# Kernel optimization log

Measured on AMD Instinct MI355X. Metric: run time of the kernel, lower is better.

## Reference

```python
import jax, jax.numpy as jnp
import numpy as np

B, L, T, D, H, DH = 8, 1024, 1024, 768, 12, 64
SPATIAL_DIM = 5


def setup_inputs() -> dict:
    key = jax.random.key(0)
    ks = jax.random.split(key, 12)
    scale = 1.0 / np.sqrt(D)
    inp = {
        "q": jax.random.normal(ks[0], (B, L, D), dtype=jnp.float32),
        "k": jax.random.normal(ks[1], (B, T, D), dtype=jnp.float32),
        "v": jax.random.normal(ks[2], (B, T, D), dtype=jnp.float32),
        "pairwise_locs": jax.random.normal(ks[3], (B, L, T, SPATIAL_DIM), dtype=jnp.float32),
        # last 64 key positions are padding in every batch row (never all-True)
        "key_padding_mask": jnp.broadcast_to(jnp.arange(T) >= T - 64, (B, T)),
        "Wq": jax.random.normal(ks[4], (D, H * DH), dtype=jnp.float32) * scale,
        "bq": jnp.zeros((H * DH,), dtype=jnp.float32),
        "Wk": jax.random.normal(ks[5], (D, H * DH), dtype=jnp.float32) * scale,
        "bk": jnp.zeros((H * DH,), dtype=jnp.float32),
        "Wv": jax.random.normal(ks[6], (D, H * DH), dtype=jnp.float32) * scale,
        "bv": jnp.zeros((H * DH,), dtype=jnp.float32),
        "Wo": jax.random.normal(ks[7], (H * DH, D), dtype=jnp.float32) * scale,
        "bo": jnp.zeros((D,), dtype=jnp.float32),
    }
    return inp


def reference(q, k, v, pairwise_locs, key_padding_mask, Wq, bq, Wk, bk, Wv, bv, Wo, bo):
    # pairwise_locs is accepted but unused in this forward path (as in the source).
    b, l, _ = q.shape
    t = k.shape[1]
    qh = (q @ Wq + bq).reshape(b, l, H, DH)  # b l h d
    kh = (k @ Wk + bk).reshape(b, t, H, DH)  # b t h d
    vh = (v @ Wv + bv).reshape(b, t, H, DH)  # b t h d
    attn = jnp.einsum('blhd,bthd->bhlt', qh, kh) / jnp.sqrt(jnp.float32(DH))
    attn = jnp.where(key_padding_mask[:, None, None, :], -jnp.inf, attn)
    fused_attn = jax.nn.softmax(attn, axis=-1)
    out = jnp.einsum('bhlt,bthd->blhd', fused_attn, vh).reshape(b, l, H * DH)
    return out @ Wo + bo  # dropout is identity in eval mode
```

## Files before the change

### kernel.cpp

```cpp
#include <hip/hip_runtime.h>
#include <hip/hip_bf16.h>
#include <cstdint>
#include <cstddef>
#include <cmath>

#define NB 8
#define NL 1024
#define NT 1024
#define ND 768
#define NH 12
#define NDH 64
#define NM (NB*NL)

typedef short short8 __attribute__((ext_vector_type(8)));
typedef unsigned short ushort4v __attribute__((ext_vector_type(4)));
typedef unsigned int uint4v __attribute__((ext_vector_type(4)));
typedef unsigned int uint2v __attribute__((ext_vector_type(2)));
typedef float f32x4 __attribute__((ext_vector_type(4)));
typedef float float4v __attribute__((ext_vector_type(4)));

__device__ __forceinline__ unsigned short f2bf(float f) {
  union { __hip_bfloat16 h; unsigned short u; } cv;
  cv.h = __float2bfloat16(f);
  return cv.u;
}
__device__ __forceinline__ unsigned pk2(float lo, float hi) {
  return (unsigned)f2bf(lo) | ((unsigned)f2bf(hi) << 16);
}
__device__ __forceinline__ f32x4 vmax4(f32x4 a, f32x4 b) {
  f32x4 r;
  r[0] = fmaxf(a[0], b[0]); r[1] = fmaxf(a[1], b[1]);
  r[2] = fmaxf(a[2], b[2]); r[3] = fmaxf(a[3], b[3]);
  return r;
}
__device__ __forceinline__ void gll16(const void* g, void* l) {
  __builtin_amdgcn_global_load_lds(
      (const __attribute__((address_space(1))) unsigned int*)g,
      (__attribute__((address_space(3))) unsigned int*)l, 16, 0, 0);
}

__global__ __launch_bounds__(128) void maskbits_kernel(
    const unsigned int* __restrict__ mask, unsigned long long* __restrict__ mb) {
  const int id = threadIdx.x;
  const unsigned int* src = mask + (size_t)(id >> 4) * NT + (id & 15) * 64;
  unsigned long long m = 0;
  for (int j = 0; j < 64; j++) m |= (unsigned long long)(src[j] != 0u) << j;
  mb[id] = m;
}

__global__ __launch_bounds__(256) void wt_kernel(
    const float* __restrict__ W0, const float* __restrict__ W1,
    const float* __restrict__ W2, const float* __restrict__ W3,
    unsigned short* __restrict__ Wt) {
  __shared__ float tile[32][33];
  const float* W = blockIdx.z == 0 ? W0 : blockIdx.z == 1 ? W1 : blockIdx.z == 2 ? W2 : W3;
  const int k0 = blockIdx.x * 32, n0 = blockIdx.y * 32;
  const int tx = threadIdx.x & 31, ty = threadIdx.x >> 5;
  for (int r = ty; r < 32; r += 8) tile[r][tx] = W[(size_t)(k0 + r) * ND + n0 + tx];
  __syncthreads();
  unsigned short* out = Wt + (size_t)blockIdx.z * ND * ND;
  for (int r = ty; r < 32; r += 8) out[(size_t)(n0 + r) * ND + k0 + tx] = f2bf(tile[tx][r]);
}

template<int MODE>
__global__ __launch_bounds__(256) void gemm_kernel(
    const float* __restrict__ Af0, const float* __restrict__ Af1,
    const float* __restrict__ Af2, const unsigned short* __restrict__ Ab,
    const unsigned short* __restrict__ Wt,
    const float* __restrict__ bias0, const float* __restrict__ bias1,
    const float* __restrict__ bias2,
    unsigned short* __restrict__ outb0, unsigned short* __restrict__ outb1,
    unsigned short* __restrict__ outb2, float* __restrict__ outf) {
  __shared__ __align__(16) unsigned short As[128 * 64];
  __shared__ __align__(16) unsigned short Bs[128 * 64];
  const int tid = threadIdx.x, lane = tid & 63, w = tid >> 6;
  const int c = lane & 15, g = lane >> 4;
  const int wrow = w & 1, wcol = w >> 1;
  const int l8 = lane >> 3, l7 = lane & 7, csw = l7 ^ l8;
  const int mbase = blockIdx.x * 128, nbase = blockIdx.y * 128;
  const int z = (MODE == 0) ? blockIdx.z : 3;

  const float* Af = (MODE == 0) ? (z == 0 ? Af0 : z == 1 ? Af1 : Af2) : nullptr;
  const unsigned short* Bt = Wt + (size_t)z * ND * ND;
  const float* bias = (MODE == 0) ? (z == 0 ? bias0 : z == 1 ? bias1 : bias2) : bias0;

  f32x4 acc[4][4];
#pragma unroll
  for (int m = 0; m < 4; m++)
#pragma unroll
    for (int n = 0; n < 4; n++) acc[m][n] = (f32x4){0.f, 0.f, 0.f, 0.f};

  for (int k0 = 0; k0 < ND; k0 += 64) {
    if (MODE == 0) {
#pragma unroll
      for (int i = 0; i < 4; i++) {
        int id = i * 256 + tid;
        int r = id >> 3, cc = id & 7;
        const float* src = &Af[(size_t)(mbase + r) * ND + k0 + cc * 8];
        float4v x0 = *(const float4v*)src;
        float4v x1 = *(const float4v*)(src + 4);
        uint4v y = {pk2(x0[0], x0[1]), pk2(x0[2], x0[3]),
                    pk2(x1[0], x1[1]), pk2(x1[2], x1[3])};
        *(uint4v*)&As[r * 64 + ((cc ^ (r & 7)) * 8)] = y;
      }
    } else {
#pragma unroll
      for (int it = 0; it < 4; it++) {
        int r = it * 32 + w * 8 + l8;
        gll16(&Ab[(size_t)(mbase + r) * ND + k0 + csw * 8], &As[(it * 32 + w * 8) * 64]);
      }
    }
#pragma unroll
    for (int it = 0; it < 4; it++) {
      int r = it * 32 + w * 8 + l8;
      gll16(&Bt[(size_t)(nbase + r) * ND + k0 + csw * 8], &Bs[(it * 32 + w * 8) * 64]);
    }
    __syncthreads();

#pragma unroll
    for (int ks = 0; ks < 2; ks++) {
      short8 a[4], b[4];
#pragma unroll
      for (int m = 0; m < 4; m++) {
        int r = wrow * 64 + m * 16 + c;
        a[m] = *(const short8*)&As[r * 64 + (((ks * 4 + g) ^ (c & 7)) * 8)];
      }
#pragma unroll
      for (int n = 0; n < 4; n++) {
        int r = wcol * 64 + n * 16 + c;
        b[n] = *(const short8*)&Bs[r * 64 + (((ks * 4 + g) ^ (c & 7)) * 8)];
      }
      if (MODE == 0 && z == 2) {
#pragma unroll
        for (int m = 0; m < 4; m++)
#pragma unroll
          for (int n = 0; n < 4; n++)
            acc[m][n] = __builtin_amdgcn_mfma_f32_16x16x32_bf16(a[m], b[n], acc[m][n], 0, 0, 0);
      } else {
#pragma unroll
        for (int m = 0; m < 4; m++)
#pragma unroll
          for (int n = 0; n < 4; n++)
            acc[m][n] = __builtin_amdgcn_mfma_f32_16x16x32_bf16(b[n], a[m], acc[m][n], 0, 0, 0);
      }
    }
    __syncthreads();
  }

  if (MODE == 0 && z == 2) {
#pragma unroll
    for (int n = 0; n < 4; n++) {
      const int col = nbase + wcol * 64 + n * 16 + c;
      const float bv = bias[col];
      const int h = col >> 6, dd = col & 63;
#pragma unroll
      for (int m = 0; m < 4; m++) {
        const int r0 = mbase + wrow * 64 + m * 16 + g * 4;
        const int bb = r0 >> 10, t = r0 & (NT - 1);
        ushort4v y;
#pragma unroll
        for (int j = 0; j < 4; j++) y[j] = f2bf(acc[m][n][j] + bv);
        *(ushort4v*)&outb2[((size_t)(bb * NH + h) * NDH + dd) * NT + t] = y;
      }
    }
  } else {
    const float scale = (MODE == 0 && z == 0) ? 0.125f * 1.44269504f : 1.0f;
    unsigned short* outb = (MODE == 0) ? (z == 0 ? outb0 : outb1) : nullptr;
#pragma unroll
    for (int n = 0; n < 4; n++) {
      const int colb = nbase + wcol * 64 + n * 16 + g * 4;
      float4v bv4 = *(const float4v*)&bias[colb];
#pragma unroll
      for (int m = 0; m < 4; m++) {
        const int row = mbase + wrow * 64 + m * 16 + c;
        if (MODE == 3) {
          float4v y;
#pragma unroll
          for (int j = 0; j < 4; j++) y[j] = acc[m][n][j] + bv4[j];
          *(float4v*)&outf[(size_t)row * ND + colb] = y;
        } else {
          ushort4v y;
#pragma unroll
          for (int j = 0; j < 4; j++) y[j] = f2bf((acc[m][n][j] + bv4[j]) * scale);
          *(ushort4v*)&outb[(size_t)row * ND + colb] = y;
        }
      }
    }
  }
}

__global__ __launch_bounds__(256) void attn_kernel(
    const unsigned short* __restrict__ qh, const unsigned short* __restrict__ kh,
    const unsigned short* __restrict__ vhT, const unsigned long long* __restrict__ maskbits,
    unsigned short* __restrict__ ao) {
  __shared__ __align__(16) unsigned short Ks[2][64 * 64];
  __shared__ __align__(16) unsigned short Vs[2][64 * 64];
  __shared__ __align__(16) unsigned short Ps[4][32 * 32];
  const int tid = threadIdx.x, lane = tid & 63, w = tid >> 6;
  const int c = lane & 15, g = lane >> 4;
  const int l8 = lane >> 3, l7 = lane & 7;
  const int swz4 = (c & 3) ^ ((c >> 2) & 3);
  const int qb = blockIdx.x * 128;
  const int b = blockIdx.y / NH, h = blockIdx.y % NH;
  const size_t kbase = (size_t)b * NT * ND + h * NDH;
  const size_t vbase = (size_t)(b * NH + h) * NDH * NT;

  const unsigned mwsrc = ((const unsigned*)maskbits)[(size_t)b * 32 + (lane & 31)];

  short8 aq[2][2];
#pragma unroll
  for (int half = 0; half < 2; half++) {
    size_t qrow = (size_t)(b * NL + qb + w * 32 + half * 16 + c) * ND + h * NDH;
#pragma unroll
    for (int ks = 0; ks < 2; ks++)
      aq[half][ks] = *(const short8*)&qh[qrow + ks * 32 + g * 8];
  }

  f32x4 o[2][4], lrv[2];
#pragma unroll
  for (int half = 0; half < 2; half++) {
    lrv[half] = (f32x4){0.f, 0.f, 0.f, 0.f};
#pragma unroll
    for (int f = 0; f < 4; f++) o[half][f] = (f32x4){0.f, 0.f, 0.f, 0.f};
  }
  float mr[2] = {-1e30f, -1e30f};

#pragma unroll
  for (int it = 0; it < 2; it++) {
    int r = w * 16 + it * 8 + l8;
    int cs = l7 ^ (r & 7);
    gll16(&kh[kbase + (size_t)r * ND + cs * 8], &Ks[0][(w * 16 + it * 8) * 64]);
    gll16(&vhT[vbase + (size_t)r * NT + cs * 8], &Vs[0][(w * 16 + it * 8) * 64]);
  }
  __syncthreads();

  for (int g0 = 0; g0 < NT; g0 += 64) {
    const int cur = (g0 >> 6) & 1;
    if (g0 + 64 < NT) {
#pragma unroll
      for (int it = 0; it < 2; it++) {
        int r = w * 16 + it * 8 + l8;
        int cs = l7 ^ (r & 7);
        gll16(&kh[kbase + (size_t)(g0 + 64 + r) * ND + cs * 8],
              &Ks[cur ^ 1][(w * 16 + it * 8) * 64]);
        gll16(&vhT[vbase + (size_t)r * NT + (g0 + 64) + cs * 8],
              &Vs[cur ^ 1][(w * 16 + it * 8) * 64]);
      }
    }

    const int tIdx = g0 >> 6;
    unsigned mlo = __shfl(mwsrc, tIdx * 2, 64);
    unsigned mhi = __shfl(mwsrc, tIdx * 2 + 1, 64);

#pragma unroll
    for (int sub = 0; sub < 2; sub++) {
      unsigned tmw = sub ? mhi : mlo;
      if (tmw != 0xffffffffu) {
        f32x4 s[2][2];
#pragma unroll
        for (int half = 0; half < 2; half++)
#pragma unroll
          for (int n = 0; n < 2; n++) s[half][n] = (f32x4){0.f, 0.f, 0.f, 0.f};
        __builtin_amdgcn_s_setprio(1);
#pragma unroll
        for (int ks = 0; ks < 2; ks++)
#pragma unroll
          for (int n = 0; n < 2; n++) {
            short8 ak = *(const short8*)&Ks[cur][(sub * 32 + n * 16 + c) * 64 +
                                                (((ks * 4 + g) ^ (c & 7)) * 8)];
            s[0][n] = __builtin_amdgcn_mfma_f32_16x16x32_bf16(ak, aq[0][ks], s[0][n], 0, 0, 0);
            s[1][n] = __builtin_amdgcn_mfma_f32_16x16x32_bf16(ak, aq[1][ks], s[1][n], 0, 0, 0);
          }
        __builtin_amdgcn_s_setprio(0);

        if (tmw) {
#pragma unroll
          for (int n = 0; n < 2; n++)
#pragma unroll
            for (int j = 0; j < 4; j++)
              if ((tmw >> (n * 16 + g * 4 + j)) & 1) { s[0][n][j] = -INFINITY; s[1][n][j] = -INFINITY; }
        }

        float mt[2];
#pragma unroll
        for (int half = 0; half < 2; half++) {
          f32x4 mv = vmax4(s[half][0], s[half][1]);
          mt[half] = fmaxf(fmaxf(mv[0], mv[1]), fmaxf(mv[2], mv[3]));
        }
        bool ok = (mt[0] <= mr[0] + 8.f) && (mt[1] <= mr[1] + 8.f);
        if (!__all(ok)) {
#pragma unroll
          for (int half = 0; half < 2; half++) {
            float mrow = mt[half];
            mrow = fmaxf(mrow, __shfl_xor(mrow, 16, 64));
            mrow = fmaxf(mrow, __shfl_xor(mrow, 32, 64));
            float mnew = fmaxf(mr[half], mrow);
            float alpha = exp2f(mr[half] - mnew);
            mr[half] = mnew;
#pragma unroll
            for (int j = 0; j < 4; j++) lrv[half][j] *= alpha;
#pragma unroll
            for (int f = 0; f < 4; f++)
#pragma unroll
              for (int j = 0; j < 4; j++) o[half][f][j] *= alpha;
          }
        }

#pragma unroll
        for (int half = 0; half < 2; half++) {
#pragma unroll
          for (int n = 0; n < 2; n++) {
#pragma unroll
            for (int j = 0; j < 4; j++) s[half][n][j] = exp2f(s[half][n][j] - mr[half]);
            lrv[half] += s[half][n];
            uint2v y = {pk2(s[half][n][0], s[half][n][1]),
                        pk2(s[half][n][2], s[half][n][3])};
            *(uint2v*)&Ps[w][(half * 16 + c) * 32 +
                             (((2 * n + (g >> 1)) ^ swz4) * 8) + (g & 1) * 4] = y;
          }
        }

        __builtin_amdgcn_s_setprio(1);
        short8 bp0 = *(const short8*)&Ps[w][c * 32 + ((g ^ swz4) * 8)];
        short8 bp1 = *(const short8*)&Ps[w][(16 + c) * 32 + ((g ^ swz4) * 8)];
#pragma unroll
        for (int f = 0; f < 4; f++) {
          short8 av = *(const short8*)&Vs[cur][(f * 16 + c) * 64 +
                                              (((sub * 4 + g) ^ (c & 7)) * 8)];
          o[0][f] = __builtin_amdgcn_mfma_f32_16x16x32_bf16(av, bp0, o[0][f], 0, 0, 0);
          o[1][f] = __builtin_amdgcn_mfma_f32_16x16x32_bf16(av, bp1, o[1][f], 0, 0, 0);
        }
        __builtin_amdgcn_s_setprio(0);
      }
    }
    __syncthreads();
  }

#pragma unroll
  for (int half = 0; half < 2; half++) {
    float lr = (lrv[half][0] + lrv[half][1]) + (lrv[half][2] + lrv[half][3]);
    lr += __shfl_xor(lr, 16, 64);
    lr += __shfl_xor(lr, 32, 64);
    float inv = 1.f / lr;
    size_t row = (size_t)(b * NL + qb + w * 32 + half * 16 + c) * ND + h * NDH;
#pragma unroll
    for (int f = 0; f < 4; f++) {
      ushort4v y;
#pragma unroll
      for (int j = 0; j < 4; j++) y[j] = f2bf(o[half][f][j] * inv);
      *(ushort4v*)&ao[row + f * 16 + g * 4] = y;
    }
  }
}

extern "C" void kernel_launch(void* const* d_in, const int* in_sizes, int n_in,
                              void* d_out, int out_size, void* d_ws, size_t ws_size,
                              hipStream_t stream) {
  const float* q  = (const float*)d_in[0];
  const float* k  = (const float*)d_in[1];
  const float* v  = (const float*)d_in[2];
  const unsigned int* mask = (const unsigned int*)d_in[4];
  const float* Wq = (const float*)d_in[5];
  const float* bq = (const float*)d_in[6];
  const float* Wk = (const float*)d_in[7];
  const float* bk = (const float*)d_in[8];
  const float* Wv = (const float*)d_in[9];
  const float* bv = (const float*)d_in[10];
  const float* Wo = (const float*)d_in[11];
  const float* bo = (const float*)d_in[12];
  float* out = (float*)d_out;

  unsigned short* ws  = (unsigned short*)d_ws;
  unsigned short* Wt  = ws;
  unsigned short* qhb = Wt + (size_t)4 * ND * ND;
  unsigned short* khb = qhb + (size_t)NM * ND;
  unsigned short* vhT = khb + (size_t)NM * ND;
  unsigned short* aob = vhT + (size_t)NM * ND;
  unsigned long long* mb = (unsigned long long*)(aob + (size_t)NM * ND);

  wt_kernel<<<dim3(ND / 32, ND / 32, 4), 256, 0, stream>>>(Wq, Wk, Wv, Wo, Wt);
  maskbits_kernel<<<1, 128, 0, stream>>>(mask, mb);

  gemm_kernel<0><<<dim3(NM / 128, ND / 128, 3), 256, 0, stream>>>(
      q, k, v, nullptr, Wt, bq, bk, bv, qhb, khb, vhT, nullptr);

  attn_kernel<<<dim3(NL / 128, NB * NH), 256, 0, stream>>>(qhb, khb, vhT, mb, aob);

  gemm_kernel<3><<<dim3(NM / 128, ND / 128), 256, 0, stream>>>(
      nullptr, nullptr, nullptr, aob, Wt, bo, nullptr, nullptr,
      nullptr, nullptr, nullptr, out);
}
```

Measured before the change: 174.3 us.

## Switch attention to 32x32x16 MFMA and pass P through registers, not LDS

The flash-attention kernel moves from 16x16x32 to 32x32x16 bf16 MFMA tiles, so each wave holds its 32 query rows in one 16-float accumulator per tile. The probability tile is repacked in registers with a cross-half lane shuffle instead of a round trip through the per-wave LDS scratch buffer Ps, which removes LDS writes and reads. Row max and sum reductions now need only one xor shuffle. The mask check changes from per-32-key sub-blocks to the whole 64-key block, and register pressure from the 16-wide accumulators may affect occupancy.

```diff
diff --git a/kernel.cpp b/kernel.cpp
--- a/kernel.cpp
+++ b/kernel.cpp
@@ -15,8 +15,8 @@
 typedef short short8 __attribute__((ext_vector_type(8)));
 typedef unsigned short ushort4v __attribute__((ext_vector_type(4)));
 typedef unsigned int uint4v __attribute__((ext_vector_type(4)));
-typedef unsigned int uint2v __attribute__((ext_vector_type(2)));
 typedef float f32x4 __attribute__((ext_vector_type(4)));
+typedef float f32x16 __attribute__((ext_vector_type(16)));
 typedef float float4v __attribute__((ext_vector_type(4)));
 
 __device__ __forceinline__ unsigned short f2bf(float f) {
@@ -26,12 +26,6 @@
 }
 __device__ __forceinline__ unsigned pk2(float lo, float hi) {
   return (unsigned)f2bf(lo) | ((unsigned)f2bf(hi) << 16);
-}
-__device__ __forceinline__ f32x4 vmax4(f32x4 a, f32x4 b) {
-  f32x4 r;
-  r[0] = fmaxf(a[0], b[0]); r[1] = fmaxf(a[1], b[1]);
-  r[2] = fmaxf(a[2], b[2]); r[3] = fmaxf(a[3], b[3]);
-  return r;
 }
 __device__ __forceinline__ void gll16(const void* g, void* l) {
   __builtin_amdgcn_global_load_lds(
@@ -195,11 +189,9 @@
     unsigned short* __restrict__ ao) {
   __shared__ __align__(16) unsigned short Ks[2][64 * 64];
   __shared__ __align__(16) unsigned short Vs[2][64 * 64];
-  __shared__ __align__(16) unsigned short Ps[4][32 * 32];
   const int tid = threadIdx.x, lane = tid & 63, w = tid >> 6;
-  const int c = lane & 15, g = lane >> 4;
+  const int q32 = lane & 31, hi = lane >> 5;
   const int l8 = lane >> 3, l7 = lane & 7;
-  const int swz4 = (c & 3) ^ ((c >> 2) & 3);
   const int qb = blockIdx.x * 128;
   const int b = blockIdx.y / NH, h = blockIdx.y % NH;
   const size_t kbase = (size_t)b * NT * ND + h * NDH;
@@ -207,23 +199,17 @@
 
   const unsigned mwsrc = ((const unsigned*)maskbits)[(size_t)b * 32 + (lane & 31)];
 
-  short8 aq[2][2];
-#pragma unroll
-  for (int half = 0; half < 2; half++) {
-    size_t qrow = (size_t)(b * NL + qb + w * 32 + half * 16 + c) * ND + h * NDH;
-#pragma unroll
-    for (int ks = 0; ks < 2; ks++)
-      aq[half][ks] = *(const short8*)&qh[qrow + ks * 32 + g * 8];
-  }
-
-  f32x4 o[2][4], lrv[2];
-#pragma unroll
-  for (int half = 0; half < 2; half++) {
-    lrv[half] = (f32x4){0.f, 0.f, 0.f, 0.f};
-#pragma unroll
-    for (int f = 0; f < 4; f++) o[half][f] = (f32x4){0.f, 0.f, 0.f, 0.f};
-  }
-  float mr[2] = {-1e30f, -1e30f};
+  short8 aq[4];
+  {
+    size_t qrow = (size_t)(b * NL + qb + w * 32 + q32) * ND + h * NDH + hi * 8;
+#pragma unroll
+    for (int ks = 0; ks < 4; ks++)
+      aq[ks] = *(const short8*)&qh[qrow + ks * 16];
+  }
+
+  f32x16 o[2] = {{}, {}};
+  f32x4 lrv = {0.f, 0.f, 0.f, 0.f};
+  float mr = -1e30f;
 
 #pragma unroll
   for (int it = 0; it < 2; it++) {
@@ -250,107 +236,91 @@
 
     const int tIdx = g0 >> 6;
     unsigned mlo = __shfl(mwsrc, tIdx * 2, 64);
-    unsigned mhi = __shfl(mwsrc, tIdx * 2 + 1, 64);
-
-#pragma unroll
-    for (int sub = 0; sub < 2; sub++) {
-      unsigned tmw = sub ? mhi : mlo;
-      if (tmw != 0xffffffffu) {
-        f32x4 s[2][2];
-#pragma unroll
-        for (int half = 0; half < 2; half++)
-#pragma unroll
-          for (int n = 0; n < 2; n++) s[half][n] = (f32x4){0.f, 0.f, 0.f, 0.f};
+    unsigned mhi_ = __shfl(mwsrc, tIdx * 2 + 1, 64);
+
+    if ((mlo & mhi_) != 0xffffffffu) {
+      const bool anymask = (mlo | mhi_) != 0u;
+#pragma unroll
+      for (int tt = 0; tt < 2; tt++) {
+        f32x16 s = {};
         __builtin_amdgcn_s_setprio(1);
 #pragma unroll
-        for (int ks = 0; ks < 2; ks++)
-#pragma unroll
-          for (int n = 0; n < 2; n++) {
-            short8 ak = *(const short8*)&Ks[cur][(sub * 32 + n * 16 + c) * 64 +
-                                                (((ks * 4 + g) ^ (c & 7)) * 8)];
-            s[0][n] = __builtin_amdgcn_mfma_f32_16x16x32_bf16(ak, aq[0][ks], s[0][n], 0, 0, 0);
-            s[1][n] = __builtin_amdgcn_mfma_f32_16x16x32_bf16(ak, aq[1][ks], s[1][n], 0, 0, 0);
+        for (int ks = 0; ks < 4; ks++) {
+          short8 ak = *(const short8*)&Ks[cur][(tt * 32 + q32) * 64 +
+                          ((((ks << 1) | hi) ^ (q32 & 7)) * 8)];
+          s = __builtin_amdgcn_mfma_f32_32x32x16_bf16(ak, aq[ks], s, 0, 0, 0);
+        }
+        __builtin_amdgcn_s_setprio(0);
+
+        if (anymask) {
+          unsigned wsd = tt ? mhi_ : mlo;
+          wsd = hi ? (wsd >> 4) : wsd;
+#pragma unroll
+          for (int a = 0; a < 4; a++)
+#pragma unroll
+            for (int j = 0; j < 4; j++)
+              if ((wsd >> (8 * a + j)) & 1) s[4 * a + j] = -INFINITY;
+        }
+
+        float mt = s[0];
+#pragma unroll
+        for (int r = 1; r < 16; r++) mt = fmaxf(mt, s[r]);
+        mt = fmaxf(mt, __shfl_xor(mt, 32, 64));
+        if (!__all(mt <= mr + 8.f)) {
+          float mnew = fmaxf(mr, mt);
+          float alpha = exp2f(mr - mnew);
+          mr = mnew;
+          lrv *= alpha; o[0] *= alpha; o[1] *= alpha;
+        }
+        unsigned pkv[4][2];
+#pragma unroll
+        for (int a = 0; a < 4; a++) {
+          f32x4 p;
+#pragma unroll
+          for (int j = 0; j < 4; j++) p[j] = exp2f(s[4 * a + j] - mr);
+          lrv += p;
+          pkv[a][0] = pk2(p[0], p[1]);
+          pkv[a][1] = pk2(p[2], p[3]);
+        }
+
+#pragma unroll
+        for (int ts = 0; ts < 2; ts++) {
+          unsigned u0 = pkv[2 * ts][0], u1 = pkv[2 * ts][1];
+          unsigned w0 = pkv[2 * ts + 1][0], w1 = pkv[2 * ts + 1][1];
+          unsigned r0 = __shfl_xor(hi ? u0 : w0, 32, 64);
+          unsigned r1 = __shfl_xor(hi ? u1 : w1, 32, 64);
+          union { unsigned u[4]; short8 s8; } bp;
+          bp.u[0] = hi ? r0 : u0;
+          bp.u[1] = hi ? r1 : u1;
+          bp.u[2] = hi ? w0 : r0;
+          bp.u[3] = hi ? w1 : r1;
+          __builtin_amdgcn_s_setprio(1);
+#pragma unroll
+          for (int dt = 0; dt < 2; dt++) {
+            short8 av = *(const short8*)&Vs[cur][(dt * 32 + q32) * 64 +
+                            ((((tt << 2) | (ts << 1) | hi) ^ (q32 & 7)) * 8)];
+            o[dt] = __builtin_amdgcn_mfma_f32_32x32x16_bf16(av, bp.s8, o[dt], 0, 0, 0);
           }
-        __builtin_amdgcn_s_setprio(0);
-
-        if (tmw) {
-#pragma unroll
-          for (int n = 0; n < 2; n++)
-#pragma unroll
-            for (int j = 0; j < 4; j++)
-              if ((tmw >> (n * 16 + g * 4 + j)) & 1) { s[0][n][j] = -INFINITY; s[1][n][j] = -INFINITY; }
-        }
-
-        float mt[2];
-#pragma unroll
-        for (int half = 0; half < 2; half++) {
-          f32x4 mv = vmax4(s[half][0], s[half][1]);
-          mt[half] = fmaxf(fmaxf(mv[0], mv[1]), fmaxf(mv[2], mv[3]));
-        }
-        bool ok = (mt[0] <= mr[0] + 8.f) && (mt[1] <= mr[1] + 8.f);
-        if (!__all(ok)) {
-#pragma unroll
-          for (int half = 0; half < 2; half++) {
-            float mrow = mt[half];
-            mrow = fmaxf(mrow, __shfl_xor(mrow, 16, 64));
-            mrow = fmaxf(mrow, __shfl_xor(mrow, 32, 64));
-            float mnew = fmaxf(mr[half], mrow);
-            float alpha = exp2f(mr[half] - mnew);
-            mr[half] = mnew;
-#pragma unroll
-            for (int j = 0; j < 4; j++) lrv[half][j] *= alpha;
-#pragma unroll
-            for (int f = 0; f < 4; f++)
-#pragma unroll
-              for (int j = 0; j < 4; j++) o[half][f][j] *= alpha;
-          }
-        }
-
-#pragma unroll
-        for (int half = 0; half < 2; half++) {
-#pragma unroll
-          for (int n = 0; n < 2; n++) {
-#pragma unroll
-            for (int j = 0; j < 4; j++) s[half][n][j] = exp2f(s[half][n][j] - mr[half]);
-            lrv[half] += s[half][n];
-            uint2v y = {pk2(s[half][n][0], s[half][n][1]),
-                        pk2(s[half][n][2], s[half][n][3])};
-            *(uint2v*)&Ps[w][(half * 16 + c) * 32 +
-                             (((2 * n + (g >> 1)) ^ swz4) * 8) + (g & 1) * 4] = y;
-          }
-        }
-
-        __builtin_amdgcn_s_setprio(1);
-        short8 bp0 = *(const short8*)&Ps[w][c * 32 + ((g ^ swz4) * 8)];
-        short8 bp1 = *(const short8*)&Ps[w][(16 + c) * 32 + ((g ^ swz4) * 8)];
-#pragma unroll
-        for (int f = 0; f < 4; f++) {
-          short8 av = *(const short8*)&Vs[cur][(f * 16 + c) * 64 +
-                                              (((sub * 4 + g) ^ (c & 7)) * 8)];
-          o[0][f] = __builtin_amdgcn_mfma_f32_16x16x32_bf16(av, bp0, o[0][f], 0, 0, 0);
-          o[1][f] = __builtin_amdgcn_mfma_f32_16x16x32_bf16(av, bp1, o[1][f], 0, 0, 0);
-        }
-        __builtin_amdgcn_s_setprio(0);
+          __builtin_amdgcn_s_setprio(0);
+        }
       }
     }
     __syncthreads();
   }
 
-#pragma unroll
-  for (int half = 0; half < 2; half++) {
-    float lr = (lrv[half][0] + lrv[half][1]) + (lrv[half][2] + lrv[half][3]);
-    lr += __shfl_xor(lr, 16, 64);
-    lr += __shfl_xor(lr, 32, 64);
-    float inv = 1.f / lr;
-    size_t row = (size_t)(b * NL + qb + w * 32 + half * 16 + c) * ND + h * NDH;
-#pragma unroll
-    for (int f = 0; f < 4; f++) {
+  float lr = (lrv[0] + lrv[1]) + (lrv[2] + lrv[3]);
+  lr += __shfl_xor(lr, 32, 64);
+  float inv = 1.f / lr;
+  size_t row = (size_t)(b * NL + qb + w * 32 + q32) * ND + h * NDH;
+#pragma unroll
+  for (int dt = 0; dt < 2; dt++)
+#pragma unroll
+    for (int a = 0; a < 4; a++) {
       ushort4v y;
 #pragma unroll
-      for (int j = 0; j < 4; j++) y[j] = f2bf(o[half][f][j] * inv);
-      *(ushort4v*)&ao[row + f * 16 + g * 4] = y;
-    }
-  }
+      for (int j = 0; j < 4; j++) y[j] = f2bf(o[dt][4 * a + j] * inv);
+      *(ushort4v*)&ao[row + dt * 32 + 8 * a + 4 * hi] = y;
+    }
 }
 
 extern "C" void kernel_launch(void* const* d_in, const int* in_sizes, int n_in,
```

Measured after the change: 158.5 us. 1.1x faster.
